# Performance work log

Hardware: AMD Instinct MI355X
Metric: run time of the kernel (lower is better)

Reference implementation:

```python
import jax, jax.numpy as jnp
import numpy as np

N, D, A, K, E = 8192, 256, 1024, 65, 4096

def setup_inputs() -> dict:
    key = jax.random.key(0)
    ks = jax.random.split(key, 8)
    s = 0.02  # linear-init scale to keep activations sane
    return {
        "embedding": jax.random.normal(ks[0], (N, D), jnp.float32),
        "data": jax.random.randint(ks[1], (E, 2), 0, N, jnp.int64),
        "Wq": jax.random.normal(ks[2], (D, A), jnp.float32) * s,
        "bq": jnp.zeros((A,), jnp.float32),
        "Wk": jax.random.normal(ks[3], (D, A), jnp.float32) * s,
        "bk": jnp.zeros((A,), jnp.float32),
        "Wv": jax.random.normal(ks[4], (D, A), jnp.float32) * s,
        "bv": jnp.zeros((A,), jnp.float32),
        "W_edge": jax.random.normal(ks[5], (K, A, A), jnp.float32) * s,
    }

def reference(embedding, data, Wq, bq, Wk, bk, Wv, bv, W_edge):
    # NodeSelfAttention: dense full attention over all N nodes
    Q = embedding @ Wq + bq            # [N, A]
    Km = embedding @ Wk + bk           # [N, A]
    V = embedding @ Wv + bv            # [N, A]
    scale = 1.0 / jnp.sqrt(jnp.float32(D))  # note: sqrt(num_feats)=sqrt(256), as in source
    scores = (Q @ Km.T) * scale        # [N, N]
    attn = jax.nn.softmax(scores, axis=-1)
    attn_emb = attn @ V                # [N, A]
    # gather edge endpoints
    h_u = attn_emb[data[:, 0]]         # [E, A]
    h_v = attn_emb[data[:, 1]]         # [E, A]
    # KWayPred: out[e,k] = h_u[e] @ W_edge[k] @ h_v[e]
    # (source computes full ExE matmul per k and takes diag; this is the
    #  equivalent O(E*K*A^2) bilinear-diag form)
    t = jnp.einsum('ed,kdf->ekf', h_u, W_edge)   # [E, K, A]
    out = jnp.einsum('ekf,ef->ek', t, h_v)       # [E, K]
    return out
```

## Files before the change

### kernel.cpp

```cpp
#include <hip/hip_runtime.h>
#include <cstdio>
#include <cstdint>

#define NTOK 8192
#define DIM  256
#define AA   1024
#define KE   65
#define EE   4096

typedef unsigned short u16;
typedef __attribute__((ext_vector_type(4))) float   f32x4;
typedef __attribute__((ext_vector_type(8))) short   bf16x8;
typedef __attribute__((ext_vector_type(8))) unsigned short u16x8;

#define DEVI __device__ __forceinline__

DEVI u16 f2bf(float f) {
  union { float f; unsigned u; } x; x.f = f;
  unsigned r = x.u + 0x7FFFu + ((x.u >> 16) & 1u);
  return (u16)(r >> 16);
}
DEVI float bf2f(u16 h) {
  union { unsigned u; float f; } x; x.u = ((unsigned)h) << 16;
  return x.f;
}

DEVI void gload16(const void* g, void* l) {
  __builtin_amdgcn_global_load_lds(
      (const __attribute__((address_space(1))) void*)g,
      (__attribute__((address_space(3))) void*)l,
      16, 0, 0);
}

DEVI void barx() {
  asm volatile("" ::: "memory");
  __builtin_amdgcn_s_barrier();
  asm volatile("" ::: "memory");
}

DEVI void stage_half(const u16* __restrict__ g0, int ld, char* dst, int tid) {
#pragma unroll
  for (int rr = 0; rr < 2; ++rr) {
    int o = rr * 8192 + (tid >> 6) * 1024 + (tid & 63) * 16;
    int q = o ^ (((o >> 7) & 7) << 4);
    gload16(g0 + (size_t)(q >> 7) * ld + ((q & 127) >> 1),
            dst + rr * 8192 + (tid >> 6) * 1024);
  }
}

DEVI void stage_t32(const u16* __restrict__ g0, int ld, char* dst, int tid) {
#pragma unroll
  for (int rr = 0; rr < 2; ++rr) {
    int o = rr * 4096 + tid * 16;
    int q = o ^ (((o >> 7) & 3) << 4);
    gload16(g0 + (size_t)(q >> 6) * ld + ((q & 63) >> 1),
            dst + rr * 4096 + (tid >> 6) * 1024);
  }
}

template<int EPI, int QMODE>
__global__ __launch_bounds__(256, 3)
void gemm4t(const u16* __restrict__ A, int lda,
            const u16* __restrict__ B, int ldb,
            int MT, int NT, int K,
            u16* __restrict__ o_s, float scale, int ldc,
            const u16* __restrict__ Hu, float* __restrict__ o_e,
            int* __restrict__ qcnt)
{
  __shared__ __align__(16) char lds[49152];
  __shared__ int s_idx;
  char* ldsA = lds;
  char* ldsB = lds + 24576;

  const int tid = threadIdx.x, lane = tid & 63, wave = tid >> 6;
  const int wm = (wave >> 1) * 64, wn = (wave & 1) * 64;
  const int KT = K >> 5;
  const int r15 = lane & 15, g16b = (lane >> 4) * 16;

  int xcc;
  asm volatile("s_getreg_b32 %0, hwreg(20, 0, 32)" : "=s"(xcc));
  xcc &= 7;
  const int MPX = MT >> 3;
  const int NQ = NT >> 3, NR = NT & 7;

  for (int dx = 0; dx < 8; ++dx) {
    const int qi = (xcc + dx) & 7;
    int per, ntb = 0, ntc = 0;
    if constexpr (QMODE == 0) {
      per = (MT * NT) >> 3;
    } else {
      ntc = NQ + (qi < NR ? 1 : 0);
      ntb = qi * NQ + (qi < NR ? qi : NR);
      per = ntc * MT;
    }
    while (true) {
      if (tid == 0) s_idx = atomicAdd(&qcnt[qi], 1);
      __syncthreads();
      const int idx = s_idx;
      __syncthreads();
      if (idx >= per) break;
      int mt, nt;
      if constexpr (QMODE == 0) {
        mt = qi * MPX + (idx % MPX); nt = idx / MPX;
      } else {
        const int srw = ntc << 3;
        const int sr = idx / srw, rem = idx - sr * srw;
        nt = ntb + (rem >> 3); mt = (sr << 3) + (rem & 7);
      }
      const int m0 = mt * 128, n0 = nt * 128;
      const u16* Ag = A + (size_t)m0 * lda;
      const u16* Bg = B + (size_t)n0 * ldb;

      f32x4 acc[4][4];
#pragma unroll
      for (int m = 0; m < 4; ++m)
#pragma unroll
        for (int n = 0; n < 4; ++n) acc[m][n] = f32x4{0.f, 0.f, 0.f, 0.f};

      stage_t32(Ag,      lda, ldsA,         tid);
      stage_t32(Bg,      ldb, ldsB,         tid);
      stage_t32(Ag + 32, lda, ldsA + 8192,  tid);
      stage_t32(Bg + 32, ldb, ldsB + 8192,  tid);
      stage_t32(Ag + 64, lda, ldsA + 16384, tid);
      stage_t32(Bg + 64, ldb, ldsB + 16384, tid);
      asm volatile("s_waitcnt vmcnt(8)" ::: "memory");
      barx();

      int bi = 0;
      for (int t = 0; t < KT; ++t) {
        const char* Ab = ldsA + bi * 8192;
        const char* Bb = ldsB + bi * 8192;
        bf16x8 a[4], b[4];
#pragma unroll
        for (int m = 0; m < 4; ++m) {
          int p = (wm + m * 16 + r15) * 64 + g16b;
          p ^= ((p >> 7) & 3) << 4;
          a[m] = *(const bf16x8*)(Ab + p);
        }
#pragma unroll
        for (int n = 0; n < 4; ++n) {
          int p = (wn + n * 16 + r15) * 64 + g16b;
          p ^= ((p >> 7) & 3) << 4;
          b[n] = *(const bf16x8*)(Bb + p);
        }
        asm volatile("s_waitcnt lgkmcnt(0)" ::: "memory");
        __builtin_amdgcn_sched_barrier(0);
        barx();
        if (t + 3 < KT) {
          stage_t32(Ag + (size_t)(t + 3) * 32, lda, ldsA + bi * 8192, tid);
          stage_t32(Bg + (size_t)(t + 3) * 32, ldb, ldsB + bi * 8192, tid);
        }
        __builtin_amdgcn_s_setprio(1);
#pragma unroll
        for (int m = 0; m < 4; ++m)
#pragma unroll
          for (int n = 0; n < 4; ++n)
            acc[m][n] = __builtin_amdgcn_mfma_f32_16x16x32_bf16(
                a[m], b[n], acc[m][n], 0, 0, 0);
        __builtin_amdgcn_s_setprio(0);
        if (t + 3 < KT)      asm volatile("s_waitcnt vmcnt(8)" ::: "memory");
        else if (t + 2 < KT) asm volatile("s_waitcnt vmcnt(4)" ::: "memory");
        else                 asm volatile("s_waitcnt vmcnt(0)" ::: "memory");
        barx();
        bi = (bi == 2) ? 0 : bi + 1;
      }

      const int rgrp = lane >> 4, cid = lane & 15;
      if constexpr (EPI == 1) {
#pragma unroll
        for (int m = 0; m < 4; ++m)
#pragma unroll
          for (int n = 0; n < 4; ++n)
#pragma unroll
            for (int j = 0; j < 4; ++j) {
              int row = m0 + wm + m * 16 + rgrp * 4 + j;
              int col = n0 + wn + n * 16 + cid;
              o_s[(size_t)row * ldc + col] = f2bf(acc[m][n][j] * scale);
            }
      } else {
        const int kidx  = n0 >> 10;
        const int dbase = (n0 & 1023) + wn;
#pragma unroll
        for (int m = 0; m < 4; ++m)
#pragma unroll
          for (int j = 0; j < 4; ++j) {
            int row = m0 + wm + m * 16 + rgrp * 4 + j;
            float p = 0.f;
#pragma unroll
            for (int n = 0; n < 4; ++n)
              p += acc[m][n][j] * bf2f(Hu[(size_t)row * AA + dbase + n * 16 + cid]);
            p += __shfl_xor(p, 1, 64);
            p += __shfl_xor(p, 2, 64);
            p += __shfl_xor(p, 4, 64);
            p += __shfl_xor(p, 8, 64);
            if (cid == 0) atomicAdd(&o_e[(size_t)row * KE + kidx], p);
          }
      }
    }
  }
}

template<int EPI, int QMODE>
__global__ __launch_bounds__(512, 2)
void gemm8(const u16* __restrict__ A, int lda,
           const u16* __restrict__ B, int ldb,
           int MT, int NT, int K,
           u16* __restrict__ o_s, float scale, int ldc,
           const u16* __restrict__ Hu, float* __restrict__ o_e,
           int* __restrict__ qcnt)
{
  __shared__ __align__(16) char lds[131072];
  __shared__ int s_next[3];
  char* ldsA = lds;
  char* ldsB = lds + 65536;

  const int tid = threadIdx.x, lane = tid & 63, wave = tid >> 6;
  const int wm = (wave >> 2) * 128;
  const int wn = (wave & 3) * 64;
  const int wnl = (wave & 1) * 64;
  const int KT = K >> 6, KT2 = KT >> 1;
  const int r15 = lane & 15, g16 = (lane >> 4) << 4;

  int xcc;
  asm volatile("s_getreg_b32 %0, hwreg(20, 0, 32)" : "=s"(xcc));
  xcc &= 7;
  const int MPX = MT >> 3;
  const int NQ = NT >> 3, NR = NT & 7;

  const char* Ab_e = ldsA +         (wm >> 7) * 16384;
  const char* Ab_o = ldsA + 32768 + (wm >> 7) * 16384;
  const char* Bb_e = ldsB +         (wn >> 7) * 16384;
  const char* Bb_o = ldsB + 32768 + (wn >> 7) * 16384;

  int dxr = 0;
  auto pop_next = [&]() {
    while (dxr < 8) {
      const int qi = (xcc + dxr) & 7;
      int per, ntb = 0, ntc = 0;
      if constexpr (QMODE == 0) {
        per = (MT * NT) >> 3;
      } else {
        ntc = NQ + (qi < NR ? 1 : 0);
        ntb = qi * NQ + (qi < NR ? qi : NR);
        per = ntc * MT;
      }
      const int idx = atomicAdd(&qcnt[qi], 1);
      if (idx < per) {
        int mt, nt;
        if constexpr (QMODE == 0) {
          mt = qi * MPX + (idx % MPX); nt = idx / MPX;
        } else {
          const int srw = ntc << 3;
          const int sr = idx / srw, rem = idx - sr * srw;
          nt = ntb + (rem >> 3); mt = (sr << 3) + (rem & 7);
        }
        s_next[0] = mt * 256; s_next[1] = nt * 256; s_next[2] = 1;
        return;
      }
      ++dxr;
    }
    s_next[2] = 0;
  };

  if (tid == 0) pop_next();
  __syncthreads();
  int m0 = s_next[0], n0 = s_next[1];
  if (!s_next[2]) return;

#define STAGE_A2(tk, h) do { const int _tk = (tk); \
    if (_tk < KT) stage_half(A + (size_t)(m0 + (h)*128) * lda + (size_t)_tk*64, lda, \
                             ldsA + (_tk & 1) * 32768 + (h) * 16384, tid); \
    else if (have_n) stage_half(A + (size_t)(m0n + (h)*128) * lda + (size_t)(_tk-KT)*64, lda, \
                                ldsA + (_tk & 1) * 32768 + (h) * 16384, tid); } while (0)
#define STAGE_B2(tk, h) do { const int _tk = (tk); \
    if (_tk < KT) stage_half(B + (size_t)(n0 + (h)*128) * ldb + (size_t)_tk*64, ldb, \
                             ldsB + (_tk & 1) * 32768 + (h) * 16384, tid); \
    else if (have_n) stage_half(B + (size_t)(n0n + (h)*128) * ldb + (size_t)(_tk-KT)*64, ldb, \
                                ldsB + (_tk & 1) * 32768 + (h) * 16384, tid); } while (0)
#define RD_A4(base, q) \
  _Pragma("unroll") for (int m = (q)*4; m < (q)*4+4; ++m) \
  _Pragma("unroll") for (int kk = 0; kk < 2; ++kk) { \
    int p = (m*16 + r15)*128 + kk*64 + g16; p ^= ((p>>7)&7)<<4; \
    a[m][kk] = *(const bf16x8*)((base) + p); }
#define RD_B2(base, q) \
  _Pragma("unroll") for (int n = (q)*2; n < (q)*2+2; ++n) \
  _Pragma("unroll") for (int kk = 0; kk < 2; ++kk) { \
    int p = (wnl + n*16 + r15)*128 + kk*64 + g16; p ^= ((p>>7)&7)<<4; \
    b[n][kk] = *(const bf16x8*)((base) + p); }
#define MM(QM, QN) do { \
  __builtin_amdgcn_s_setprio(1); \
  _Pragma("unroll") for (int kk = 0; kk < 2; ++kk) \
  _Pragma("unroll") for (int m = 0; m < 4; ++m) \
  _Pragma("unroll") for (int n = 0; n < 2; ++n) \
    acc[(QM)*4+m][(QN)*2+n] = __builtin_amdgcn_mfma_f32_16x16x32_bf16( \
        a[(QM)*4+m][kk], b[(QN)*2+n][kk], acc[(QM)*4+m][(QN)*2+n], 0, 0, 0); \
  __builtin_amdgcn_s_setprio(0); } while (0)
#define WAIT_LGKM0 do { asm volatile("s_waitcnt lgkmcnt(0)" ::: "memory"); \
                        __builtin_amdgcn_sched_barrier(0); } while (0)
#define KTILE(t, AB, BB) do { \
    RD_B2(BB, 0); RD_A4(AB, 0); \
    STAGE_B2((t) + 1, 1); \
    asm volatile("s_waitcnt lgkmcnt(8)" ::: "memory"); \
    barx(); WAIT_LGKM0; \
    MM(0, 0); \
    barx(); \
    RD_B2(BB, 1); \
    barx(); WAIT_LGKM0; \
    MM(0, 1); \
    barx(); \
    RD_A4(AB, 1); \
    STAGE_B2((t) + 2, 0); \
    barx(); WAIT_LGKM0; \
    MM(1, 1); \
    barx(); \
    STAGE_A2((t) + 2, 0); \
    STAGE_A2((t) + 2, 1); \
    barx(); \
    __builtin_amdgcn_sched_barrier(0); \
    MM(1, 0); \
    if (vm6) asm volatile("s_waitcnt vmcnt(6)" ::: "memory"); \
    else     asm volatile("s_waitcnt vmcnt(0)" ::: "memory"); \
    barx(); } while (0)

  {
    const int m0n = 0, n0n = 0; const bool have_n = false; (void)m0n; (void)n0n; (void)have_n;
    STAGE_A2(0, 0); STAGE_A2(0, 1); STAGE_B2(0, 0); STAGE_B2(0, 1);
    STAGE_B2(1, 0); STAGE_A2(1, 0); STAGE_A2(1, 1);
  }
  asm volatile("s_waitcnt vmcnt(6)" ::: "memory");
  barx();

  while (true) {
    f32x4 acc[8][4];
#pragma unroll
    for (int m = 0; m < 8; ++m)
#pragma unroll
      for (int n = 0; n < 4; ++n) acc[m][n] = f32x4{0.f, 0.f, 0.f, 0.f};

    int m0n = 0, n0n = 0;
    bool have_n = false;

    for (int i = 0; i < KT2; ++i) {
      const int ta = 2 * i, tb = 2 * i + 1;
      if (i == KT2 - 2 && tid == 0) pop_next();
      if (i == KT2 - 1) { m0n = s_next[0]; n0n = s_next[1]; have_n = (s_next[2] != 0); }
      const bool tail = (i == KT2 - 1);
      const bool vm6 = !tail || have_n;
      bf16x8 a[8][2], b[4][2];
      KTILE(ta, Ab_e, Bb_e);
      KTILE(tb, Ab_o, Bb_o);
    }

    const int rgrp = lane >> 4, cid = lane & 15;
    if constexpr (EPI == 1) {
#pragma unroll
      for (int m = 0; m < 8; ++m)
#pragma unroll
        for (int n = 0; n < 4; ++n)
#pragma unroll
          for (int j = 0; j < 4; ++j) {
            int row = m0 + wm + m * 16 + rgrp * 4 + j;
            int col = n0 + wn + n * 16 + cid;
            o_s[(size_t)row * ldc + col] = f2bf(acc[m][n][j] * scale);
          }
    } else {
      const int kidx  = n0 >> 10;
      const int dbase = (n0 & 1023) + wn;
#pragma unroll
      for (int m = 0; m < 8; ++m)
#pragma unroll
        for (int j = 0; j < 4; ++j) {
          int row = m0 + wm + m * 16 + rgrp * 4 + j;
          float p = 0.f;
#pragma unroll
          for (int n = 0; n < 4; ++n)
            p += acc[m][n][j] * bf2f(Hu[(size_t)row * AA + dbase + n * 16 + cid]);
          p += __shfl_xor(p, 1, 64);
          p += __shfl_xor(p, 2, 64);
          p += __shfl_xor(p, 4, 64);
          p += __shfl_xor(p, 8, 64);
          if (cid == 0) atomicAdd(&o_e[(size_t)row * KE + kidx], p);
        }
    }

    if (!have_n) break;
    m0 = m0n; n0 = n0n;
  }
#undef STAGE_A2
#undef STAGE_B2
#undef RD_A4
#undef RD_B2
#undef MM
#undef WAIT_LGKM0
#undef KTILE
}

#define BM 128
#define BN 128
#define BK 64

template<int EPI, bool BF32>
__global__ __launch_bounds__(256)
void gemm_bt(const u16* __restrict__ A, int lda,
             const void* __restrict__ Bptr, int ldb,
             int MT, int NT, int K,
             u16* __restrict__ o_q, u16* __restrict__ o_k, u16* __restrict__ o_vt,
             const float* __restrict__ biasc,
             u16* __restrict__ o_s, float scale, int ldc,
             const u16* __restrict__ Hu, float* __restrict__ o_e)
{
  const int nb  = MT * NT;
  const int per = nb >> 3;
  int bid = blockIdx.x;
  bid = (bid & 7) * per + (bid >> 3);
  const int mt = bid % MT, nt = bid / MT;
  const int m0 = mt * BM, n0 = nt * BN;

  __shared__ u16 As[BM * BK];
  __shared__ u16 Bs[BN * BK];

  const int tid  = threadIdx.x;
  const int lane = tid & 63, wave = tid >> 6;
  const int wm = (wave >> 1) * 64, wn = (wave & 1) * 64;

  f32x4 acc[4][4];
#pragma unroll
  for (int m = 0; m < 4; ++m)
#pragma unroll
    for (int n = 0; n < 4; ++n) acc[m][n] = f32x4{0.f, 0.f, 0.f, 0.f};

  const u16*   Bh = (const u16*)Bptr;
  const float* Bf = (const float*)Bptr;

  const int KT = K / BK;
  for (int kt = 0; kt < KT; ++kt) {
    const int k0 = kt * BK;
#pragma unroll
    for (int it = 0; it < 4; ++it) {
      int o = it * 4096 + wave * 1024 + lane * 16;
      int r = o >> 7;
      int c = (o & 127) >> 1;
      gload16(A + (size_t)(m0 + r) * lda + k0 + c,
              &As[(it * 4096 + wave * 1024) >> 1]);
    }
    if constexpr (!BF32) {
#pragma unroll
      for (int it = 0; it < 4; ++it) {
        int o = it * 4096 + wave * 1024 + lane * 16;
        int r = o >> 7;
        int c = (o & 127) >> 1;
        gload16(Bh + (size_t)(n0 + r) * ldb + k0 + c,
                &Bs[(it * 4096 + wave * 1024) >> 1]);
      }
    } else {
#pragma unroll
      for (int it = 0; it < 8; ++it) {
        int e = it * 1024 + tid * 4;
        int r = e >> 6, c = e & 63;
        const float4 v = *(const float4*)(Bf + (size_t)(n0 + r) * ldb + k0 + c);
        ushort4 h;
        h.x = f2bf(v.x); h.y = f2bf(v.y); h.z = f2bf(v.z); h.w = f2bf(v.w);
        *(ushort4*)&Bs[r * BK + c] = h;
      }
    }
    asm volatile("s_waitcnt vmcnt(0)" ::: "memory");
    __syncthreads();

#pragma unroll
    for (int kk = 0; kk < 2; ++kk) {
      const int ro = lane & 15;
      const int ko = kk * 32 + (lane >> 4) * 8;
      bf16x8 af[4], bfg[4];
#pragma unroll
      for (int m = 0; m < 4; ++m)
        af[m] = *(const bf16x8*)&As[(wm + m * 16 + ro) * BK + ko];
#pragma unroll
      for (int n = 0; n < 4; ++n)
        bfg[n] = *(const bf16x8*)&Bs[(wn + n * 16 + ro) * BK + ko];
#pragma unroll
      for (int m = 0; m < 4; ++m)
#pragma unroll
        for (int n = 0; n < 4; ++n)
          acc[m][n] = __builtin_amdgcn_mfma_f32_16x16x32_bf16(
              af[m], bfg[n], acc[m][n], 0, 0, 0);
    }
    __syncthreads();
  }

  const int rgrp = lane >> 4, cid = lane & 15;

  if constexpr (EPI == 0) {
#pragma unroll
    for (int m = 0; m < 4; ++m)
#pragma unroll
      for (int n = 0; n < 4; ++n)
#pragma unroll
        for (int j = 0; j < 4; ++j) {
          int row = m0 + wm + m * 16 + rgrp * 4 + j;
          int col = n0 + wn + n * 16 + cid;
          float v = acc[m][n][j] + biasc[col];
          u16 h = f2bf(v);
          if (col < 1024)       o_q[(size_t)row * AA + col] = h;
          else if (col < 2048)  o_k[(size_t)row * AA + (col - 1024)] = h;
          else                  o_vt[(size_t)(col - 2048) * NTOK + row] = h;
        }
  } else if constexpr (EPI == 1) {
#pragma unroll
    for (int m = 0; m < 4; ++m)
#pragma unroll
      for (int n = 0; n < 4; ++n)
#pragma unroll
        for (int j = 0; j < 4; ++j) {
          int row = m0 + wm + m * 16 + rgrp * 4 + j;
          int col = n0 + wn + n * 16 + cid;
          o_s[(size_t)row * ldc + col] = f2bf(acc[m][n][j] * scale);
        }
  } else {
    const int kidx  = n0 >> 10;
    const int dbase = (n0 & 1023) + wn;
#pragma unroll
    for (int m = 0; m < 4; ++m)
#pragma unroll
      for (int j = 0; j < 4; ++j) {
        int row = m0 + wm + m * 16 + rgrp * 4 + j;
        float p = 0.f;
#pragma unroll
        for (int n = 0; n < 4; ++n) {
          int d = dbase + n * 16 + cid;
          p += acc[m][n][j] * bf2f(Hu[(size_t)row * AA + d]);
        }
        p += __shfl_xor(p, 1, 64);
        p += __shfl_xor(p, 2, 64);
        p += __shfl_xor(p, 4, 64);
        p += __shfl_xor(p, 8, 64);
        if (cid == 0) atomicAdd(&o_e[(size_t)row * KE + kidx], p);
      }
  }
}

__global__ __launch_bounds__(256)
void softmax_rows(u16* __restrict__ S)
{
  const size_t base = (size_t)blockIdx.x * 8192;
  const int tid = threadIdx.x;
  const int lane = tid & 63, wave = tid >> 6;
  float v[32];
#pragma unroll
  for (int c = 0; c < 4; ++c) {
    u16x8 u = *(const u16x8*)&S[base + c * 2048 + tid * 8];
#pragma unroll
    for (int j = 0; j < 8; ++j) v[c * 8 + j] = bf2f(u[j]);
  }
  float mx = -1e30f;
#pragma unroll
  for (int i = 0; i < 32; ++i) mx = fmaxf(mx, v[i]);
#pragma unroll
  for (int off = 1; off < 64; off <<= 1) mx = fmaxf(mx, __shfl_xor(mx, off, 64));
  __shared__ float r1[4], r2[4];
  if (lane == 0) r1[wave] = mx;
  __syncthreads();
  mx = fmaxf(fmaxf(r1[0], r1[1]), fmaxf(r1[2], r1[3]));

  float s = 0.f;
#pragma unroll
  for (int i = 0; i < 32; ++i) { v[i] = __expf(v[i] - mx); s += v[i]; }
#pragma unroll
  for (int off = 1; off < 64; off <<= 1) s += __shfl_xor(s, off, 64);
  if (lane == 0) r2[wave] = s;
  __syncthreads();
  s = r2[0] + r2[1] + r2[2] + r2[3];
  const float inv = 1.f / s;
#pragma unroll
  for (int c = 0; c < 4; ++c) {
    u16x8 u;
#pragma unroll
    for (int j = 0; j < 8; ++j) u[j] = f2bf(v[c * 8 + j] * inv);
    *(u16x8*)&S[base + c * 2048 + tid * 8] = u;
  }
}

__global__ __launch_bounds__(256)
void gather_rows(const unsigned* __restrict__ dw, const u16* __restrict__ AE,
                 u16* __restrict__ Hu, u16* __restrict__ Hv)
{
  bool i64 = true;
#pragma unroll
  for (int w = 1; w < 32; w += 2) i64 = i64 && (dw[w] == 0u);
  const int e = blockIdx.x;
  const unsigned iu = i64 ? dw[4 * e]     : dw[2 * e];
  const unsigned iv = i64 ? dw[4 * e + 2] : dw[2 * e + 1];
  const int t = threadIdx.x;
  *(ushort4*)&Hu[(size_t)e * AA + t * 4] = *(const ushort4*)&AE[(size_t)iu * AA + t * 4];
  *(ushort4*)&Hv[(size_t)e * AA + t * 4] = *(const ushort4*)&AE[(size_t)iv * AA + t * 4];
}

__global__ __launch_bounds__(256)
void init_misc(float* __restrict__ out_e, const float* __restrict__ bq,
               const float* __restrict__ bk, const float* __restrict__ bv,
               float* __restrict__ biasc, int* __restrict__ qall)
{
  const int i = blockIdx.x * 256 + threadIdx.x;
  if (i < EE * KE) out_e[i] = 0.f;
  if (i < 1024) {
    biasc[i]        = bq[i];
    biasc[1024 + i] = bk[i];
    biasc[2048 + i] = bv[i];
  }
  if (i < 64) qall[i] = 0;
}

__global__ __launch_bounds__(256)
void cvt_f32_bf16_v4(const float* __restrict__ src, u16* __restrict__ dst, int n4)
{
  for (int i = blockIdx.x * 256 + threadIdx.x; i < n4; i += gridDim.x * 256) {
    float4 v = ((const float4*)src)[i];
    ushort4 h; h.x = f2bf(v.x); h.y = f2bf(v.y); h.z = f2bf(v.z); h.w = f2bf(v.w);
    ((ushort4*)dst)[i] = h;
  }
}

__global__ __launch_bounds__(256)
void build_wT(const float* __restrict__ Wq, const float* __restrict__ Wk,
              const float* __restrict__ Wv, u16* __restrict__ WT)
{
  const int nn = blockIdx.x;
  const int d  = threadIdx.x;
  const float* W = (nn < 1024) ? Wq : ((nn < 2048) ? Wk : Wv);
  WT[nn * DIM + d] = f2bf(W[(size_t)d * AA + (nn & 1023)]);
}

extern "C" void kernel_launch(void* const* d_in, const int* in_sizes, int n_in,
                              void* d_out, int out_size, void* d_ws, size_t ws_size,
                              hipStream_t stream)
{
  (void)in_sizes; (void)out_size;
  if (n_in < 9) return;
  const float*    emb  = (const float*)d_in[0];
  const unsigned* data = (const unsigned*)d_in[1];
  const float* Wq = (const float*)d_in[2];
  const float* bq = (const float*)d_in[3];
  const float* Wk = (const float*)d_in[4];
  const float* bk = (const float*)d_in[5];
  const float* Wv = (const float*)d_in[6];
  const float* bv = (const float*)d_in[7];
  const float* We = (const float*)d_in[8];
  float* out = (float*)d_out;

  char* ws = (char*)d_ws;
  size_t off = 0;
  auto alloc = [&](size_t bytes) -> void* {
    void* p = ws + off;
    off += (bytes + 255) & ~(size_t)255;
    return p;
  };
  u16*   emb_b = (u16*)alloc((size_t)NTOK * DIM * 2);
  u16*   WT    = (u16*)alloc((size_t)3072 * DIM * 2);
  float* biasc = (float*)alloc(3072 * 4);
  int*   qall  = (int*)alloc(64 * 4);
  u16*   Qb    = (u16*)alloc((size_t)NTOK * AA * 2);
  u16*   Kb    = (u16*)alloc((size_t)NTOK * AA * 2);
  u16*   Vt    = (u16*)alloc((size_t)AA * NTOK * 2);
  u16*   AE    = (u16*)alloc((size_t)NTOK * AA * 2);
  u16*   Hu    = (u16*)alloc((size_t)EE * AA * 2);
  u16*   Hv    = (u16*)alloc((size_t)EE * AA * 2);

  const size_t webf_bytes = ((size_t)KE * AA * AA * 2 + 255) & ~(size_t)255;
  u16* We_b = nullptr;
  if (off + webf_bytes + (size_t)1024 * NTOK * 2 <= ws_size) {
    We_b = (u16*)(ws + off);
    off += webf_bytes;
  }

  int chunk = 4096;
  while (chunk > 128 && off + (size_t)chunk * NTOK * 2 > ws_size) chunk >>= 1;
  u16* Sc = (u16*)alloc((size_t)chunk * NTOK * 2);
  if (off > ws_size) {
    fprintf(stderr, "kernel_launch: ws too small (need %zu, have %zu)\n", off, ws_size);
    return;
  }

  init_misc<<<(EE * KE) / 256, 256, 0, stream>>>(out, bq, bk, bv, biasc, qall);
  cvt_f32_bf16_v4<<<2048, 256, 0, stream>>>(emb, emb_b, NTOK * DIM / 4);
  build_wT<<<3072, 256, 0, stream>>>(Wq, Wk, Wv, WT);
  if (We_b)
    cvt_f32_bf16_v4<<<4096, 256, 0, stream>>>(We, We_b, KE * AA * AA / 4);

  gemm_bt<0, false><<<64 * 24, 256, 0, stream>>>(
      emb_b, DIM, WT, DIM, 64, 24, DIM,
      Qb, Kb, Vt, biasc, nullptr, 0.f, 0, nullptr, nullptr);

  const int nch = NTOK / chunk;
  for (int ci = 0; ci < nch; ++ci) {
    const u16* Qc = Qb + (size_t)ci * chunk * AA;
    const bool big = ((chunk & 2047) == 0);
    if (big)
      gemm8<1, 1><<<256, 512, 0, stream>>>(
          Qc, AA, Kb, AA, chunk / 256, 32, AA,
          Sc, 0.0625f, NTOK, nullptr, nullptr, qall + 8 * ci);
    else
      gemm_bt<1, false><<<(chunk / 128) * 64, 256, 0, stream>>>(
          Qc, AA, Kb, AA, chunk / 128, 64, AA,
          nullptr, nullptr, nullptr, nullptr, Sc, 0.0625f, NTOK, nullptr, nullptr);
    softmax_rows<<<chunk, 256, 0, stream>>>(Sc);
    if (big)
      gemm4t<1, 1><<<768, 256, 0, stream>>>(
          Sc, NTOK, Vt, NTOK, chunk / 128, 8, NTOK,
          AE + (size_t)ci * chunk * AA, 1.0f, AA, nullptr, nullptr,
          qall + 16 + 8 * ci);
    else
      gemm_bt<1, false><<<(chunk / 128) * 8, 256, 0, stream>>>(
          Sc, NTOK, Vt, NTOK, chunk / 128, 8, NTOK,
          nullptr, nullptr, nullptr, nullptr,
          AE + (size_t)ci * chunk * AA, 1.0f, AA, nullptr, nullptr);
  }

  gather_rows<<<EE, 256, 0, stream>>>(data, AE, Hu, Hv);

  if (We_b)
    gemm4t<2, 1><<<768, 256, 0, stream>>>(
        Hv, AA, We_b, AA, 32, 520, AA,
        nullptr, 0.f, 0, Hu, out, qall + 32);
  else
    gemm_bt<3, true><<<32 * 520, 256, 0, stream>>>(
        Hv, AA, We, AA, 32, 520, AA,
        nullptr, nullptr, nullptr, nullptr, nullptr, 0.f, 0, Hu, out);
}
```

Baseline: 1.579 ms.

## Widen edge-bilinear GEMM tile to 256x128 with double buffering; use gemm_bt for attn@V

The persistent 4-wave GEMM now computes a 256x128 tile, with each wave holding 128x64 (8x4 MFMA accumulators), and drops from triple to double buffering. It runs at two blocks per CU. It is used only for the final W_edge bilinear product, which halves the M tile count and doubles reuse of each W_edge tile loaded. The attn@V GEMM in the big-chunk path switches from the persistent queue kernel to the plain gemm_bt kernel. The costs are more register pressure, lower occupancy and a shallower prefetch depth.

```diff
diff --git a/kernel.cpp b/kernel.cpp
--- a/kernel.cpp
+++ b/kernel.cpp
@@ -59,8 +59,8 @@
 }
 
 template<int EPI, int QMODE>
-__global__ __launch_bounds__(256, 3)
-void gemm4t(const u16* __restrict__ A, int lda,
+__global__ __launch_bounds__(256, 2)
+void gemm4n(const u16* __restrict__ A, int lda,
             const u16* __restrict__ B, int ldb,
             int MT, int NT, int K,
             u16* __restrict__ o_s, float scale, int ldc,
@@ -70,10 +70,11 @@
   __shared__ __align__(16) char lds[49152];
   __shared__ int s_idx;
   char* ldsA = lds;
-  char* ldsB = lds + 24576;
+  char* ldsB = lds + 32768;
 
   const int tid = threadIdx.x, lane = tid & 63, wave = tid >> 6;
-  const int wm = (wave >> 1) * 64, wn = (wave & 1) * 64;
+  const int wm = (wave >> 1) * 128;
+  const int wn = (wave & 1) * 64;
   const int KT = K >> 5;
   const int r15 = lane & 15, g16b = (lane >> 4) * 16;
 
@@ -82,6 +83,10 @@
   xcc &= 7;
   const int MPX = MT >> 3;
   const int NQ = NT >> 3, NR = NT & 7;
+
+#define STAGE_A32(tk, buf) do { const u16* _g = Ag + (size_t)(tk) * 32; \
+    stage_t32(_g,                      lda, (buf),        tid); \
+    stage_t32(_g + (size_t)128 * lda,  lda, (buf) + 8192, tid); } while (0)
 
   for (int dx = 0; dx < 8; ++dx) {
     const int qi = (xcc + dx) & 7;
@@ -105,70 +110,69 @@
       } else {
         const int srw = ntc << 3;
         const int sr = idx / srw, rem = idx - sr * srw;
-        nt = ntb + (rem >> 3); mt = (sr << 3) + (rem & 7);
+        nt = ntb + (rem >> 3);
+        mt = (sr << 3) + (rem & 7);
       }
-      const int m0 = mt * 128, n0 = nt * 128;
+      const int m0 = mt * 256, n0 = nt * 128;
       const u16* Ag = A + (size_t)m0 * lda;
       const u16* Bg = B + (size_t)n0 * ldb;
 
-      f32x4 acc[4][4];
-#pragma unroll
-      for (int m = 0; m < 4; ++m)
+      f32x4 acc[8][4];
+#pragma unroll
+      for (int m = 0; m < 8; ++m)
 #pragma unroll
         for (int n = 0; n < 4; ++n) acc[m][n] = f32x4{0.f, 0.f, 0.f, 0.f};
 
-      stage_t32(Ag,      lda, ldsA,         tid);
-      stage_t32(Bg,      ldb, ldsB,         tid);
-      stage_t32(Ag + 32, lda, ldsA + 8192,  tid);
-      stage_t32(Bg + 32, ldb, ldsB + 8192,  tid);
-      stage_t32(Ag + 64, lda, ldsA + 16384, tid);
-      stage_t32(Bg + 64, ldb, ldsB + 16384, tid);
-      asm volatile("s_waitcnt vmcnt(8)" ::: "memory");
+      STAGE_A32(0, ldsA);
+      stage_t32(Bg, ldb, ldsB, tid);
+      STAGE_A32(1, ldsA + 16384);
+      stage_t32(Bg + 32, ldb, ldsB + 8192, tid);
+      asm volatile("s_waitcnt vmcnt(6)" ::: "memory");
       barx();
 
-      int bi = 0;
       for (int t = 0; t < KT; ++t) {
-        const char* Ab = ldsA + bi * 8192;
-        const char* Bb = ldsB + bi * 8192;
-        bf16x8 a[4], b[4];
-#pragma unroll
-        for (int m = 0; m < 4; ++m) {
-          int p = (wm + m * 16 + r15) * 64 + g16b;
+        const int par = t & 1;
+        const char* Ab = ldsA + par * 16384;
+        const char* Bb = ldsB + par * 8192;
+        bf16x8 a[8], b[4];
+#pragma unroll
+        for (int m = 0; m < 8; ++m) {
+          const int lr = wm + m * 16 + r15;
+          int p = (lr & 127) * 64 + g16b;
           p ^= ((p >> 7) & 3) << 4;
-          a[m] = *(const bf16x8*)(Ab + p);
+          a[m] = *(const bf16x8*)(Ab + (lr >> 7) * 8192 + p);
         }
 #pragma unroll
         for (int n = 0; n < 4; ++n) {
-          int p = (wn + n * 16 + r15) * 64 + g16b;
+          const int lr = wn + n * 16 + r15;
+          int p = lr * 64 + g16b;
           p ^= ((p >> 7) & 3) << 4;
           b[n] = *(const bf16x8*)(Bb + p);
         }
         asm volatile("s_waitcnt lgkmcnt(0)" ::: "memory");
         __builtin_amdgcn_sched_barrier(0);
         barx();
-        if (t + 3 < KT) {
-          stage_t32(Ag + (size_t)(t + 3) * 32, lda, ldsA + bi * 8192, tid);
-          stage_t32(Bg + (size_t)(t + 3) * 32, ldb, ldsB + bi * 8192, tid);
+        if (t + 2 < KT) {
+          STAGE_A32(t + 2, ldsA + par * 16384);
+          stage_t32(Bg + (size_t)(t + 2) * 32, ldb, ldsB + par * 8192, tid);
         }
         __builtin_amdgcn_s_setprio(1);
 #pragma unroll
-        for (int m = 0; m < 4; ++m)
+        for (int m = 0; m < 8; ++m)
 #pragma unroll
           for (int n = 0; n < 4; ++n)
             acc[m][n] = __builtin_amdgcn_mfma_f32_16x16x32_bf16(
                 a[m], b[n], acc[m][n], 0, 0, 0);
         __builtin_amdgcn_s_setprio(0);
-        if (t + 3 < KT)      asm volatile("s_waitcnt vmcnt(8)" ::: "memory");
-        else if (t + 2 < KT) asm volatile("s_waitcnt vmcnt(4)" ::: "memory");
-        else                 asm volatile("s_waitcnt vmcnt(0)" ::: "memory");
+        if (t + 2 < KT) asm volatile("s_waitcnt vmcnt(6)" ::: "memory");
+        else            asm volatile("s_waitcnt vmcnt(0)" ::: "memory");
         barx();
-        bi = (bi == 2) ? 0 : bi + 1;
       }
 
       const int rgrp = lane >> 4, cid = lane & 15;
       if constexpr (EPI == 1) {
 #pragma unroll
-        for (int m = 0; m < 4; ++m)
+        for (int m = 0; m < 8; ++m)
 #pragma unroll
           for (int n = 0; n < 4; ++n)
 #pragma unroll
@@ -181,7 +185,7 @@
         const int kidx  = n0 >> 10;
         const int dbase = (n0 & 1023) + wn;
 #pragma unroll
-        for (int m = 0; m < 4; ++m)
+        for (int m = 0; m < 8; ++m)
 #pragma unroll
           for (int j = 0; j < 4; ++j) {
             int row = m0 + wm + m * 16 + rgrp * 4 + j;
@@ -198,6 +202,7 @@
       }
     }
   }
+#undef STAGE_A32
 }
 
 template<int EPI, int QMODE>
@@ -702,23 +707,17 @@
           Qc, AA, Kb, AA, chunk / 128, 64, AA,
           nullptr, nullptr, nullptr, nullptr, Sc, 0.0625f, NTOK, nullptr, nullptr);
     softmax_rows<<<chunk, 256, 0, stream>>>(Sc);
-    if (big)
-      gemm4t<1, 1><<<768, 256, 0, stream>>>(
-          Sc, NTOK, Vt, NTOK, chunk / 128, 8, NTOK,
-          AE + (size_t)ci * chunk * AA, 1.0f, AA, nullptr, nullptr,
-          qall + 16 + 8 * ci);
-    else
-      gemm_bt<1, false><<<(chunk / 128) * 8, 256, 0, stream>>>(
-          Sc, NTOK, Vt, NTOK, chunk / 128, 8, NTOK,
-          nullptr, nullptr, nullptr, nullptr,
-          AE + (size_t)ci * chunk * AA, 1.0f, AA, nullptr, nullptr);
+    gemm_bt<1, false><<<(chunk / 128) * 8, 256, 0, stream>>>(
+        Sc, NTOK, Vt, NTOK, chunk / 128, 8, NTOK,
+        nullptr, nullptr, nullptr, nullptr,
+        AE + (size_t)ci * chunk * AA, 1.0f, AA, nullptr, nullptr);
   }
 
   gather_rows<<<EE, 256, 0, stream>>>(data, AE, Hu, Hv);
 
   if (We_b)
-    gemm4t<2, 1><<<768, 256, 0, stream>>>(
-        Hv, AA, We_b, AA, 32, 520, AA,
+    gemm4n<2, 1><<<512, 256, 0, stream>>>(
+        Hv, AA, We_b, AA, 16, 520, AA,
         nullptr, 0.f, 0, Hu, out, qall + 32);
   else
     gemm_bt<3, true><<<32 * 520, 256, 0, stream>>>(
```

Result: faster. 1.496 ms (-5.2%).
